# Kernel tuning notes

Measured on AMD Instinct MI355X. Metric: run time of the kernel, lower is better.

Reference implementation:

```python
import jax, jax.numpy as jnp
import numpy as np

B, N, K = 2, 1280, 48
C_NODE, C_EDGE, C_OUT = 384, 128, 128
C_BIAS = C_NODE // 2          # 192 (node_dilation=2)
HID = 2 * C_BIAS + C_EDGE     # 512
LN_EPS = 1e-5


def setup_inputs() -> dict:
    key = jax.random.key(0)
    ks = jax.random.split(key, 13)
    w = lambda k, shape: (jax.random.normal(k, shape, jnp.float32) * 0.02)
    return {
        "node_emb": jax.random.normal(ks[0], (B, N, C_NODE), jnp.float32),
        "edge_emb": jax.random.normal(ks[1], (B, N, K, C_EDGE), jnp.float32),
        "E_idx": jax.random.randint(ks[2], (B, N, K), 0, N),
        "Wi": w(ks[3], (C_NODE, C_BIAS)), "bi": jnp.zeros((C_BIAS,), jnp.float32),
        "W1": w(ks[4], (HID, HID)), "b1": jnp.zeros((HID,), jnp.float32),
        "W2": w(ks[5], (HID, HID)), "b2": jnp.zeros((HID,), jnp.float32),
        "Wf": w(ks[6], (HID, C_OUT)), "bf": jnp.zeros((C_OUT,), jnp.float32),
        "gamma": jnp.ones((C_OUT,), jnp.float32),
        "beta": jnp.zeros((C_OUT,), jnp.float32),
    }


def reference(node_emb, edge_emb, E_idx, Wi, bi, W1, b1, W2, b2, Wf, bf, gamma, beta):
    # initial_embed: [B, N, C_NODE] -> [B, N, C_BIAS]
    n = node_emb @ Wi + bi
    # edge_bias[b,i,k] = concat(n[b,i], n[b, E_idx[b,i,k]])  (tile + gather_edges fused)
    nbr = jax.vmap(lambda v, e: v[e])(n, E_idx)                     # [B, N, K, C_BIAS]
    slf = jnp.broadcast_to(n[:, :, None, :], nbr.shape)             # [B, N, K, C_BIAS]
    x = jnp.concatenate([edge_emb, slf, nbr], axis=-1)              # [B, N, K, HID]
    h = jax.nn.relu(x @ W1 + b1)
    h = jax.nn.relu(h @ W2 + b2)
    # final_layer on residual sum, then LayerNorm
    y = (h + x) @ Wf + bf                                           # [B, N, K, C_OUT]
    mu = jnp.mean(y, axis=-1, keepdims=True)
    var = jnp.mean((y - mu) ** 2, axis=-1, keepdims=True)
    return (y - mu) * jax.lax.rsqrt(var + LN_EPS) * gamma + beta
```

## Files before the change

### kernel.cpp

```cpp
#include <hip/hip_runtime.h>
#include <stdint.h>

#define BB    2
#define NN    1280
#define KK    48
#define CN    384
#define CE    128
#define CB    192
#define HID   512
#define CO    128
#define MM    (BB*NN*KK)
#define CH    (MM/2)

typedef __bf16 bf16x8 __attribute__((ext_vector_type(8)));
typedef float  f32x4  __attribute__((ext_vector_type(4)));
typedef unsigned short u16x8 __attribute__((ext_vector_type(8)));

__device__ __forceinline__ unsigned short f2bf(float f) {
  unsigned int i = __builtin_bit_cast(unsigned int, f);
  unsigned int r = (i + 0x7fffu + ((i >> 16) & 1u)) >> 16;
  return (unsigned short)r;
}
__device__ __forceinline__ float bf2f(unsigned short u) {
  unsigned int v = ((unsigned int)u) << 16;
  return __builtin_bit_cast(float, v);
}

__device__ __forceinline__ void gload_lds16(const void* g, void* l) {
  __builtin_amdgcn_global_load_lds(
      (const __attribute__((address_space(1))) void*)g,
      (__attribute__((address_space(3))) void*)l, 16, 0, 0);
}

__device__ __forceinline__ void mfma_tiles(const char* ldsA, const char* ldsB,
                                           int l, int wm, int wn,
                                           f32x4 (&acc)[4][4]) {
#pragma unroll
  for (int kk = 0; kk < 2; ++kk) {
    bf16x8 av[4], bv[4];
#pragma unroll
    for (int t = 0; t < 4; ++t) {
      const int ra = wm * 64 + t * 16 + (l & 15);
      const int ca = (kk * 4 + (l >> 4)) ^ (ra & 7);
      av[t] = *(const bf16x8*)(ldsA + ra * 128 + ca * 16);
      const int rb = wn * 64 + t * 16 + (l & 15);
      const int cb = (kk * 4 + (l >> 4)) ^ (rb & 7);
      bv[t] = *(const bf16x8*)(ldsB + rb * 128 + cb * 16);
    }
#pragma unroll
    for (int mt = 0; mt < 4; ++mt)
#pragma unroll
      for (int nt = 0; nt < 4; ++nt)
        acc[mt][nt] = __builtin_amdgcn_mfma_f32_16x16x32_bf16(av[mt], bv[nt], acc[mt][nt], 0, 0, 0);
  }
}

__global__ void k_transpose_cast(const float* __restrict__ in,
                                 unsigned short* __restrict__ out,
                                 int R, int C) {
  __shared__ float tile[32][33];
  const int c0 = blockIdx.x * 32, r0 = blockIdx.y * 32;
  const int tx = threadIdx.x, ty = threadIdx.y;
#pragma unroll
  for (int dy = 0; dy < 32; dy += 8)
    tile[ty + dy][tx] = in[(size_t)(r0 + ty + dy) * C + c0 + tx];
  __syncthreads();
#pragma unroll
  for (int dy = 0; dy < 32; dy += 8)
    out[(size_t)(c0 + ty + dy) * R + r0 + tx] = f2bf(tile[tx][ty + dy]);
}

__global__ void k_node(const float* __restrict__ node,
                       const float* __restrict__ Wi,
                       const float* __restrict__ bi,
                       unsigned short* __restrict__ nbuf) {
  __shared__ float row[CN];
  const int blk = blockIdx.x;
  const float* src = node + (size_t)blk * CN;
  for (int c = threadIdx.x; c < CN; c += CB) row[c] = src[c];
  __syncthreads();
  const int t = threadIdx.x;
  float acc = bi[t];
#pragma unroll 8
  for (int c = 0; c < CN; ++c) acc += row[c] * Wi[(size_t)c * CB + t];
  nbuf[(size_t)blk * CB + t] = f2bf(acc);
}

__global__ __launch_bounds__(256, 2)
void k_gemm1(const float* __restrict__ edge,
             const unsigned short* __restrict__ nbuf,
             const int* __restrict__ eidx,
             const unsigned short* __restrict__ Wt,
             const float* __restrict__ bias,
             unsigned short* __restrict__ out,
             int mbase, int b) {
  __shared__ char lds[32768];
  char* ldsA = lds;
  char* ldsB = lds + 16384;
  const int flat = blockIdx.x;
  const int xcd = flat & 7;
  const int p = flat >> 3;
  const int m0 = (xcd * 60 + (p >> 2)) * 128;
  const int n0 = (p & 3) * 128;
  const int tid = threadIdx.x;
  const int l = tid & 63;
  const int w = tid >> 6;
  const int wm = w >> 1, wn = w & 1;
  const int sr = l >> 3, pc = l & 7;
  const int lc = pc ^ sr;

  int rr[4], big[4], nbrg[4];
  size_t mg[4];
#pragma unroll
  for (int ii = 0; ii < 4; ++ii) {
    const int r = (w * 4 + ii) * 8 + sr;
    rr[ii] = r;
    const int m = mbase + m0 + r;
    mg[ii] = (size_t)m;
    big[ii] = m / KK;
    nbrg[ii] = b * NN + eidx[m];
  }

  f32x4 acc[4][4];
#pragma unroll
  for (int i = 0; i < 4; ++i)
#pragma unroll
    for (int j = 0; j < 4; ++j) acc[i][j] = (f32x4){0.f, 0.f, 0.f, 0.f};

#pragma unroll
  for (int k0 = 0; k0 < HID; k0 += 64) {
    uint4 rga[4];
    if (k0 < 128) {
#pragma unroll
      for (int ii = 0; ii < 4; ++ii) {
        const float4* ep = (const float4*)(edge + mg[ii] * CE + k0 + lc * 8);
        float4 x0 = ep[0], x1 = ep[1];
        u16x8 pk;
        pk[0] = f2bf(x0.x); pk[1] = f2bf(x0.y); pk[2] = f2bf(x0.z); pk[3] = f2bf(x0.w);
        pk[4] = f2bf(x1.x); pk[5] = f2bf(x1.y); pk[6] = f2bf(x1.z); pk[7] = f2bf(x1.w);
        rga[ii] = __builtin_bit_cast(uint4, pk);
      }
    }
    __syncthreads();
#pragma unroll
    for (int ii = 0; ii < 4; ++ii) {
      const int i = w * 4 + ii;
      gload_lds16(Wt + (size_t)(n0 + rr[ii]) * HID + k0 + lc * 8, ldsB + i * 1024);
      if (k0 < 128) {
        *(uint4*)(ldsA + i * 1024 + l * 16) = rga[ii];
      } else if (k0 < 320) {
        gload_lds16(nbuf + (size_t)big[ii] * CB + (k0 - 128) + lc * 8, ldsA + i * 1024);
      } else {
        gload_lds16(nbuf + (size_t)nbrg[ii] * CB + (k0 - 320) + lc * 8, ldsA + i * 1024);
      }
    }
    __syncthreads();
    mfma_tiles(ldsA, ldsB, l, wm, wn, acc);
  }

  __syncthreads();
  unsigned short* tile = (unsigned short*)lds;
  const int q = l >> 4, cc = l & 15;
#pragma unroll
  for (int nt = 0; nt < 4; ++nt) {
    const int col = wn * 64 + nt * 16 + cc;
    const float bvv = bias[n0 + col];
    const int cn = col >> 3, cb = col & 7;
#pragma unroll
    for (int mt = 0; mt < 4; ++mt) {
      const int r0_ = wm * 64 + mt * 16 + q * 4;
#pragma unroll
      for (int r = 0; r < 4; ++r) {
        float v = acc[mt][nt][r] + bvv;
        v = v > 0.f ? v : 0.f;
        const int row = r0_ + r;
        tile[row * 128 + ((cn ^ (row & 7)) << 3) + cb] = f2bf(v);
      }
    }
  }
  __syncthreads();
#pragma unroll
  for (int i = 0; i < 8; ++i) {
    const int c = i * 256 + tid;
    const int row = c >> 4, cn = c & 15;
    u16x8 vv = *(const u16x8*)(tile + row * 128 + ((cn ^ (row & 7)) << 3));
    *(u16x8*)(out + (size_t)(m0 + row) * HID + n0 + cn * 8) = vv;
  }
}

__global__ __launch_bounds__(256, 2)
void k_gemm2(const unsigned short* __restrict__ A,
             const unsigned short* __restrict__ Wt,
             const float* __restrict__ bias,
             const float* __restrict__ edge,
             const unsigned short* __restrict__ nbuf,
             const int* __restrict__ eidx,
             unsigned short* __restrict__ out,
             int mbase, int b) {
  __shared__ char lds[32768];
  char* ldsA = lds;
  char* ldsB = lds + 16384;
  const int flat = blockIdx.x;
  const int xcd = flat & 7;
  const int p = flat >> 3;
  const int m0 = (xcd * 60 + (p >> 2)) * 128;
  const int n0 = (p & 3) * 128;
  const int tid = threadIdx.x;
  const int l = tid & 63;
  const int w = tid >> 6;
  const int wm = w >> 1, wn = w & 1;
  const int sr = l >> 3, pc = l & 7;
  const int lc = pc ^ sr;

  f32x4 acc[4][4];
#pragma unroll
  for (int i = 0; i < 4; ++i)
#pragma unroll
    for (int j = 0; j < 4; ++j) acc[i][j] = (f32x4){0.f, 0.f, 0.f, 0.f};

#pragma unroll
  for (int k0 = 0; k0 < HID; k0 += 64) {
    __syncthreads();
#pragma unroll
    for (int ii = 0; ii < 4; ++ii) {
      const int i = w * 4 + ii;
      const int r = i * 8 + sr;
      gload_lds16(A  + (size_t)(m0 + r) * HID + k0 + lc * 8, ldsA + i * 1024);
      gload_lds16(Wt + (size_t)(n0 + r) * HID + k0 + lc * 8, ldsB + i * 1024);
    }
    __syncthreads();
    mfma_tiles(ldsA, ldsB, l, wm, wn, acc);
  }

  __syncthreads();
  unsigned short* tile = (unsigned short*)lds;
  const int q = l >> 4, cc = l & 15;
#pragma unroll
  for (int nt = 0; nt < 4; ++nt) {
    const int col = wn * 64 + nt * 16 + cc;
    const float bvv = bias[n0 + col];
    const int cn = col >> 3, cb = col & 7;
#pragma unroll
    for (int mt = 0; mt < 4; ++mt) {
      const int r0_ = wm * 64 + mt * 16 + q * 4;
#pragma unroll
      for (int r = 0; r < 4; ++r) {
        float v = acc[mt][nt][r] + bvv;
        v = v > 0.f ? v : 0.f;
        const int row = r0_ + r;
        tile[row * 128 + ((cn ^ (row & 7)) << 3) + cb] = f2bf(v);
      }
    }
  }
  __syncthreads();
#pragma unroll
  for (int i = 0; i < 8; ++i) {
    const int c = i * 256 + tid;
    const int row = c >> 4, cn = c & 15;
    u16x8 vv = *(const u16x8*)(tile + row * 128 + ((cn ^ (row & 7)) << 3));
    const int m = mbase + m0 + row;
    float rv[8];
    if (n0 == 0) {
      const float4* ep = (const float4*)(edge + (size_t)m * CE + cn * 8);
      float4 x0 = ep[0], x1 = ep[1];
      rv[0] = x0.x; rv[1] = x0.y; rv[2] = x0.z; rv[3] = x0.w;
      rv[4] = x1.x; rv[5] = x1.y; rv[6] = x1.z; rv[7] = x1.w;
    } else if (n0 == 128) {
      u16x8 xv = *(const u16x8*)(nbuf + (size_t)(m / KK) * CB + cn * 8);
#pragma unroll
      for (int j = 0; j < 8; ++j) rv[j] = bf2f(xv[j]);
    } else if (n0 == 256) {
      u16x8 xv;
      if (cn < 8) {
        xv = *(const u16x8*)(nbuf + (size_t)(m / KK) * CB + 128 + cn * 8);
      } else {
        const int e = eidx[m];
        xv = *(const u16x8*)(nbuf + (size_t)(b * NN + e) * CB + cn * 8 - 64);
      }
#pragma unroll
      for (int j = 0; j < 8; ++j) rv[j] = bf2f(xv[j]);
    } else {
      const int e = eidx[m];
      u16x8 xv = *(const u16x8*)(nbuf + (size_t)(b * NN + e) * CB + 64 + cn * 8);
#pragma unroll
      for (int j = 0; j < 8; ++j) rv[j] = bf2f(xv[j]);
    }
#pragma unroll
    for (int j = 0; j < 8; ++j) vv[j] = f2bf(bf2f(vv[j]) + rv[j]);
    *(u16x8*)(out + (size_t)(m0 + row) * HID + n0 + cn * 8) = vv;
  }
}

__global__ __launch_bounds__(256, 2)
void k_final(const unsigned short* __restrict__ A,
             const unsigned short* __restrict__ Wft,
             const float* __restrict__ bias,
             const float* __restrict__ gamma,
             const float* __restrict__ beta,
             float* __restrict__ out) {
  __shared__ char lds[32768];
  char* ldsA = lds;
  char* ldsB = lds + 16384;
  const int m0 = blockIdx.x * 128;
  const int tid = threadIdx.x;
  const int l = tid & 63;
  const int w = tid >> 6;
  const int sr = l >> 3, pc = l & 7;
  const int lc = pc ^ sr;

  f32x4 acc[2][8];
#pragma unroll
  for (int i = 0; i < 2; ++i)
#pragma unroll
    for (int j = 0; j < 8; ++j) acc[i][j] = (f32x4){0.f, 0.f, 0.f, 0.f};

#pragma unroll
  for (int k0 = 0; k0 < HID; k0 += 64) {
    __syncthreads();
#pragma unroll
    for (int ii = 0; ii < 4; ++ii) {
      const int i = w * 4 + ii;
      const int r = i * 8 + sr;
      gload_lds16(A   + (size_t)(m0 + r) * HID + k0 + lc * 8, ldsA + i * 1024);
      gload_lds16(Wft + (size_t)r * HID + k0 + lc * 8,        ldsB + i * 1024);
    }
    __syncthreads();
#pragma unroll
    for (int kk = 0; kk < 2; ++kk) {
      bf16x8 av[2], bv[8];
#pragma unroll
      for (int t = 0; t < 2; ++t) {
        const int ra = w * 32 + t * 16 + (l & 15);
        const int ca = (kk * 4 + (l >> 4)) ^ (ra & 7);
        av[t] = *(const bf16x8*)(ldsA + ra * 128 + ca * 16);
      }
#pragma unroll
      for (int t = 0; t < 8; ++t) {
        const int rb = t * 16 + (l & 15);
        const int cb = (kk * 4 + (l >> 4)) ^ (rb & 7);
        bv[t] = *(const bf16x8*)(ldsB + rb * 128 + cb * 16);
      }
#pragma unroll
      for (int mt = 0; mt < 2; ++mt)
#pragma unroll
        for (int nt = 0; nt < 8; ++nt)
          acc[mt][nt] = __builtin_amdgcn_mfma_f32_16x16x32_bf16(av[mt], bv[nt], acc[mt][nt], 0, 0, 0);
    }
  }

  const int q = l >> 4, cc = l & 15;
  float gg[8], bb[8], bs[8];
#pragma unroll
  for (int j = 0; j < 8; ++j) {
    const int col = j * 16 + cc;
    gg[j] = gamma[col];
    bb[j] = beta[col];
    bs[j] = bias[col];
  }
#pragma unroll
  for (int mt = 0; mt < 2; ++mt) {
#pragma unroll
    for (int r = 0; r < 4; ++r) {
      float s = 0.f, ss = 0.f;
#pragma unroll
      for (int j = 0; j < 8; ++j) {
        const float v = acc[mt][j][r] + bs[j];
        acc[mt][j][r] = v;
        s += v;
        ss += v * v;
      }
#pragma unroll
      for (int mk = 1; mk < 16; mk <<= 1) {
        s  += __shfl_xor(s, mk, 64);
        ss += __shfl_xor(ss, mk, 64);
      }
      const float mu = s * (1.f / 128.f);
      const float var = ss * (1.f / 128.f) - mu * mu;
      const float rstd = rsqrtf(var + 1e-5f);
      const int row = m0 + w * 32 + mt * 16 + q * 4 + r;
#pragma unroll
      for (int j = 0; j < 8; ++j) {
        const float v = (acc[mt][j][r] - mu) * rstd * gg[j] + bb[j];
        out[(size_t)row * CO + j * 16 + cc] = v;
      }
    }
  }
}

#define O_N    ((size_t)0)
#define O_WT1  ((size_t)0x100000)
#define O_WT2  (O_WT1 + (size_t)0x80000)
#define O_WFT  (O_WT2 + (size_t)0x80000)
#define O_H1   ((size_t)0x300000)
#define O_A    (O_H1 + (size_t)CH * HID * 2)

extern "C" void kernel_launch(void* const* d_in, const int* in_sizes, int n_in,
                              void* d_out, int out_size, void* d_ws, size_t ws_size,
                              hipStream_t stream) {
  const float* node  = (const float*)d_in[0];
  const float* edge  = (const float*)d_in[1];
  const int*   eidx  = (const int*)d_in[2];
  const float* Wi    = (const float*)d_in[3];
  const float* bi    = (const float*)d_in[4];
  const float* W1    = (const float*)d_in[5];
  const float* b1    = (const float*)d_in[6];
  const float* W2    = (const float*)d_in[7];
  const float* b2    = (const float*)d_in[8];
  const float* Wf    = (const float*)d_in[9];
  const float* bfv   = (const float*)d_in[10];
  const float* gamma = (const float*)d_in[11];
  const float* beta  = (const float*)d_in[12];
  float* out = (float*)d_out;

  char* ws = (char*)d_ws;
  unsigned short* nbuf = (unsigned short*)(ws + O_N);
  unsigned short* Wt1  = (unsigned short*)(ws + O_WT1);
  unsigned short* Wt2  = (unsigned short*)(ws + O_WT2);
  unsigned short* Wft  = (unsigned short*)(ws + O_WFT);
  unsigned short* h1   = (unsigned short*)(ws + O_H1);
  unsigned short* abuf = (unsigned short*)(ws + O_A);

  k_transpose_cast<<<dim3(HID / 32, HID / 32), dim3(32, 8), 0, stream>>>(W1, Wt1, HID, HID);
  k_transpose_cast<<<dim3(HID / 32, HID / 32), dim3(32, 8), 0, stream>>>(W2, Wt2, HID, HID);
  k_transpose_cast<<<dim3(CO / 32, HID / 32), dim3(32, 8), 0, stream>>>(Wf, Wft, HID, CO);

  k_node<<<BB * NN, CB, 0, stream>>>(node, Wi, bi, nbuf);

  for (int c = 0; c < 2; ++c) {
    k_gemm1<<<(CH / 128) * 4, 256, 0, stream>>>(edge, nbuf, eidx, Wt1, b1, h1, c * CH, c);
    k_gemm2<<<(CH / 128) * 4, 256, 0, stream>>>(h1, Wt2, b2, edge, nbuf, eidx, abuf, c * CH, c);
    k_final<<<CH / 128, 256, 0, stream>>>(abuf, Wft, bfv, gamma, beta, out + (size_t)c * CH * CO);
  }
}
```

Measured before the change: 394.7 us.

## Double-buffer LDS tiles in all three GEMM kernels to overlap loads with MFMA

Each GEMM kernel now uses two 32KB LDS buffers. The next K-slice is prefetched with direct-to-LDS global loads, plus register loads for the fp32 edge slice in gemm1, while MFMAs run on the current buffer. This cuts the two barriers per K step to one and hides global load latency behind compute. In exchange, LDS per block grows to 64KB, which can reduce occupancy relative to the launch_bounds target of 2 blocks per CU.

```diff
diff --git a/kernel.cpp b/kernel.cpp
--- a/kernel.cpp
+++ b/kernel.cpp
@@ -94,9 +94,7 @@
              const float* __restrict__ bias,
              unsigned short* __restrict__ out,
              int mbase, int b) {
-  __shared__ char lds[32768];
-  char* ldsA = lds;
-  char* ldsB = lds + 16384;
+  __shared__ char lds[65536];
   const int flat = blockIdx.x;
   const int xcd = flat & 7;
   const int p = flat >> 3;
@@ -128,37 +126,59 @@
     for (int j = 0; j < 4; ++j) acc[i][j] = (f32x4){0.f, 0.f, 0.f, 0.f};
 
 #pragma unroll
-  for (int k0 = 0; k0 < HID; k0 += 64) {
-    uint4 rga[4];
-    if (k0 < 128) {
+  for (int ii = 0; ii < 4; ++ii) {
+    const int i = w * 4 + ii;
+    gload_lds16(Wt + (size_t)(n0 + rr[ii]) * HID + lc * 8, lds + 16384 + i * 1024);
+    const float4* ep = (const float4*)(edge + mg[ii] * CE + lc * 8);
+    float4 x0 = ep[0], x1 = ep[1];
+    u16x8 pk;
+    pk[0] = f2bf(x0.x); pk[1] = f2bf(x0.y); pk[2] = f2bf(x0.z); pk[3] = f2bf(x0.w);
+    pk[4] = f2bf(x1.x); pk[5] = f2bf(x1.y); pk[6] = f2bf(x1.z); pk[7] = f2bf(x1.w);
+    *(uint4*)(lds + i * 1024 + l * 16) = __builtin_bit_cast(uint4, pk);
+  }
+  __syncthreads();
+
+#pragma unroll
+  for (int t = 0; t < 8; ++t) {
+    char* base_c = lds + (t & 1) * 32768;
+    char* base_n = lds + ((t & 1) ^ 1) * 32768;
+    const int kn = (t + 1) * 64;
+    float4 e0[4], e1[4];
+    if (t < 7) {
 #pragma unroll
       for (int ii = 0; ii < 4; ++ii) {
-        const float4* ep = (const float4*)(edge + mg[ii] * CE + k0 + lc * 8);
-        float4 x0 = ep[0], x1 = ep[1];
+        const int i = w * 4 + ii;
+        gload_lds16(Wt + (size_t)(n0 + rr[ii]) * HID + kn + lc * 8,
+                    base_n + 16384 + i * 1024);
+        if (kn < 128) {
+          const float4* ep = (const float4*)(edge + mg[ii] * CE + kn + lc * 8);
+          e0[ii] = ep[0];
+          e1[ii] = ep[1];
+        } else if (kn < 320) {
+          gload_lds16(nbuf + (size_t)big[ii] * CB + (kn - 128) + lc * 8,
+                      base_n + i * 1024);
+        } else {
+          gload_lds16(nbuf + (size_t)nbrg[ii] * CB + (kn - 320) + lc * 8,
+                      base_n + i * 1024);
+        }
+      }
+    }
+    mfma_tiles(base_c, base_c + 16384, l, wm, wn, acc);
+    if (t < 7 && kn < 128) {
+#pragma unroll
+      for (int ii = 0; ii < 4; ++ii) {
+        const int i = w * 4 + ii;
         u16x8 pk;
-        pk[0] = f2bf(x0.x); pk[1] = f2bf(x0.y); pk[2] = f2bf(x0.z); pk[3] = f2bf(x0.w);
-        pk[4] = f2bf(x1.x); pk[5] = f2bf(x1.y); pk[6] = f2bf(x1.z); pk[7] = f2bf(x1.w);
-        rga[ii] = __builtin_bit_cast(uint4, pk);
+        pk[0] = f2bf(e0[ii].x); pk[1] = f2bf(e0[ii].y);
+        pk[2] = f2bf(e0[ii].z); pk[3] = f2bf(e0[ii].w);
+        pk[4] = f2bf(e1[ii].x); pk[5] = f2bf(e1[ii].y);
+        pk[6] = f2bf(e1[ii].z); pk[7] = f2bf(e1[ii].w);
+        *(uint4*)(base_n + i * 1024 + l * 16) = __builtin_bit_cast(uint4, pk);
       }
     }
     __syncthreads();
-#pragma unroll
-    for (int ii = 0; ii < 4; ++ii) {
-      const int i = w * 4 + ii;
-      gload_lds16(Wt + (size_t)(n0 + rr[ii]) * HID + k0 + lc * 8, ldsB + i * 1024);
-      if (k0 < 128) {
-        *(uint4*)(ldsA + i * 1024 + l * 16) = rga[ii];
-      } else if (k0 < 320) {
-        gload_lds16(nbuf + (size_t)big[ii] * CB + (k0 - 128) + lc * 8, ldsA + i * 1024);
-      } else {
-        gload_lds16(nbuf + (size_t)nbrg[ii] * CB + (k0 - 320) + lc * 8, ldsA + i * 1024);
-      }
-    }
-    __syncthreads();
-    mfma_tiles(ldsA, ldsB, l, wm, wn, acc);
-  }
-
-  __syncthreads();
+  }
+
   unsigned short* tile = (unsigned short*)lds;
   const int q = l >> 4, cc = l & 15;
 #pragma unroll
@@ -197,9 +217,7 @@
              const int* __restrict__ eidx,
              unsigned short* __restrict__ out,
              int mbase, int b) {
-  __shared__ char lds[32768];
-  char* ldsA = lds;
-  char* ldsB = lds + 16384;
+  __shared__ char lds[65536];
   const int flat = blockIdx.x;
   const int xcd = flat & 7;
   const int p = flat >> 3;
@@ -219,20 +237,32 @@
     for (int j = 0; j < 4; ++j) acc[i][j] = (f32x4){0.f, 0.f, 0.f, 0.f};
 
 #pragma unroll
-  for (int k0 = 0; k0 < HID; k0 += 64) {
+  for (int ii = 0; ii < 4; ++ii) {
+    const int i = w * 4 + ii;
+    const int r = i * 8 + sr;
+    gload_lds16(A  + (size_t)(m0 + r) * HID + lc * 8, lds + i * 1024);
+    gload_lds16(Wt + (size_t)(n0 + r) * HID + lc * 8, lds + 16384 + i * 1024);
+  }
+  __syncthreads();
+
+#pragma unroll
+  for (int t = 0; t < 8; ++t) {
+    char* base_c = lds + (t & 1) * 32768;
+    char* base_n = lds + ((t & 1) ^ 1) * 32768;
+    const int kn = (t + 1) * 64;
+    if (t < 7) {
+#pragma unroll
+      for (int ii = 0; ii < 4; ++ii) {
+        const int i = w * 4 + ii;
+        const int r = i * 8 + sr;
+        gload_lds16(A  + (size_t)(m0 + r) * HID + kn + lc * 8, base_n + i * 1024);
+        gload_lds16(Wt + (size_t)(n0 + r) * HID + kn + lc * 8, base_n + 16384 + i * 1024);
+      }
+    }
+    mfma_tiles(base_c, base_c + 16384, l, wm, wn, acc);
     __syncthreads();
-#pragma unroll
-    for (int ii = 0; ii < 4; ++ii) {
-      const int i = w * 4 + ii;
-      const int r = i * 8 + sr;
-      gload_lds16(A  + (size_t)(m0 + r) * HID + k0 + lc * 8, ldsA + i * 1024);
-      gload_lds16(Wt + (size_t)(n0 + r) * HID + k0 + lc * 8, ldsB + i * 1024);
-    }
-    __syncthreads();
-    mfma_tiles(ldsA, ldsB, l, wm, wn, acc);
-  }
-
-  __syncthreads();
+  }
+
   unsigned short* tile = (unsigned short*)lds;
   const int q = l >> 4, cc = l & 15;
 #pragma unroll
@@ -298,9 +328,7 @@
              const float* __restrict__ gamma,
              const float* __restrict__ beta,
              float* __restrict__ out) {
-  __shared__ char lds[32768];
-  char* ldsA = lds;
-  char* ldsB = lds + 16384;
+  __shared__ char lds[65536];
   const int m0 = blockIdx.x * 128;
   const int tid = threadIdx.x;
   const int l = tid & 63;
@@ -315,30 +343,43 @@
     for (int j = 0; j < 8; ++j) acc[i][j] = (f32x4){0.f, 0.f, 0.f, 0.f};
 
 #pragma unroll
-  for (int k0 = 0; k0 < HID; k0 += 64) {
-    __syncthreads();
-#pragma unroll
-    for (int ii = 0; ii < 4; ++ii) {
-      const int i = w * 4 + ii;
-      const int r = i * 8 + sr;
-      gload_lds16(A   + (size_t)(m0 + r) * HID + k0 + lc * 8, ldsA + i * 1024);
-      gload_lds16(Wft + (size_t)r * HID + k0 + lc * 8,        ldsB + i * 1024);
-    }
-    __syncthreads();
+  for (int ii = 0; ii < 4; ++ii) {
+    const int i = w * 4 + ii;
+    const int r = i * 8 + sr;
+    gload_lds16(A   + (size_t)(m0 + r) * HID + lc * 8, lds + i * 1024);
+    gload_lds16(Wft + (size_t)r * HID + lc * 8,        lds + 16384 + i * 1024);
+  }
+  __syncthreads();
+
+#pragma unroll
+  for (int t = 0; t < 8; ++t) {
+    char* ldsA = lds + (t & 1) * 32768;
+    char* ldsB = ldsA + 16384;
+    char* base_n = lds + ((t & 1) ^ 1) * 32768;
+    const int kn = (t + 1) * 64;
+    if (t < 7) {
+#pragma unroll
+      for (int ii = 0; ii < 4; ++ii) {
+        const int i = w * 4 + ii;
+        const int r = i * 8 + sr;
+        gload_lds16(A   + (size_t)(m0 + r) * HID + kn + lc * 8, base_n + i * 1024);
+        gload_lds16(Wft + (size_t)r * HID + kn + lc * 8,        base_n + 16384 + i * 1024);
+      }
+    }
 #pragma unroll
     for (int kk = 0; kk < 2; ++kk) {
       bf16x8 av[2], bv[8];
 #pragma unroll
-      for (int t = 0; t < 2; ++t) {
-        const int ra = w * 32 + t * 16 + (l & 15);
+      for (int tt = 0; tt < 2; ++tt) {
+        const int ra = w * 32 + tt * 16 + (l & 15);
         const int ca = (kk * 4 + (l >> 4)) ^ (ra & 7);
-        av[t] = *(const bf16x8*)(ldsA + ra * 128 + ca * 16);
-      }
-#pragma unroll
-      for (int t = 0; t < 8; ++t) {
-        const int rb = t * 16 + (l & 15);
+        av[tt] = *(const bf16x8*)(ldsA + ra * 128 + ca * 16);
+      }
+#pragma unroll
+      for (int tt = 0; tt < 8; ++tt) {
+        const int rb = tt * 16 + (l & 15);
         const int cb = (kk * 4 + (l >> 4)) ^ (rb & 7);
-        bv[t] = *(const bf16x8*)(ldsB + rb * 128 + cb * 16);
+        bv[tt] = *(const bf16x8*)(ldsB + rb * 128 + cb * 16);
       }
 #pragma unroll
       for (int mt = 0; mt < 2; ++mt)
@@ -346,6 +387,7 @@
         for (int nt = 0; nt < 8; ++nt)
           acc[mt][nt] = __builtin_amdgcn_mfma_f32_16x16x32_bf16(av[mt], bv[nt], acc[mt][nt], 0, 0, 0);
     }
+    __syncthreads();
   }
 
   const int q = l >> 4, cc = l & 15;
```

Measured after the change: 422.2 us. +7.0%, slower.

## Restructure GEMMs to keep A rows in registers and whole B panel in LDS

Applied to the files above, without the earlier changes.

All three GEMM kernels are rewritten so each wave loads its A-operand rows directly from global memory into registers for the full K=512, and the block's whole 64-column weight panel is staged into 64 KB of LDS once, with a single barrier. This removes the per-K-step sync/reload loop. The final kernel reads weights straight from global memory with no LDS. Tile shapes change to 64x64 (gemm1), 128x64 (gemm2) and 64-row final blocks, and grids grow to match. The risk is heavy register pressure (up to 32 bf16x8 A fragments) and 64 KB LDS limiting occupancy, plus less reuse of A across N tiles.

```diff
diff --git a/kernel.cpp b/kernel.cpp
--- a/kernel.cpp
+++ b/kernel.cpp
@@ -32,29 +32,6 @@
       (__attribute__((address_space(3))) void*)l, 16, 0, 0);
 }
 
-__device__ __forceinline__ void mfma_tiles(const char* ldsA, const char* ldsB,
-                                           int l, int wm, int wn,
-                                           f32x4 (&acc)[4][4]) {
-#pragma unroll
-  for (int kk = 0; kk < 2; ++kk) {
-    bf16x8 av[4], bv[4];
-#pragma unroll
-    for (int t = 0; t < 4; ++t) {
-      const int ra = wm * 64 + t * 16 + (l & 15);
-      const int ca = (kk * 4 + (l >> 4)) ^ (ra & 7);
-      av[t] = *(const bf16x8*)(ldsA + ra * 128 + ca * 16);
-      const int rb = wn * 64 + t * 16 + (l & 15);
-      const int cb = (kk * 4 + (l >> 4)) ^ (rb & 7);
-      bv[t] = *(const bf16x8*)(ldsB + rb * 128 + cb * 16);
-    }
-#pragma unroll
-    for (int mt = 0; mt < 4; ++mt)
-#pragma unroll
-      for (int nt = 0; nt < 4; ++nt)
-        acc[mt][nt] = __builtin_amdgcn_mfma_f32_16x16x32_bf16(av[mt], bv[nt], acc[mt][nt], 0, 0, 0);
-  }
-}
-
 __global__ void k_transpose_cast(const float* __restrict__ in,
                                  unsigned short* __restrict__ out,
                                  int R, int C) {
@@ -86,6 +63,7 @@
   nbuf[(size_t)blk * CB + t] = f2bf(acc);
 }
 
+
 __global__ __launch_bounds__(256, 2)
 void k_gemm1(const float* __restrict__ edge,
              const unsigned short* __restrict__ nbuf,
@@ -94,96 +72,96 @@
              const float* __restrict__ bias,
              unsigned short* __restrict__ out,
              int mbase, int b) {
-  __shared__ char lds[32768];
-  char* ldsA = lds;
-  char* ldsB = lds + 16384;
+  __shared__ char lds[65536];
   const int flat = blockIdx.x;
   const int xcd = flat & 7;
   const int p = flat >> 3;
-  const int m0 = (xcd * 60 + (p >> 2)) * 128;
-  const int n0 = (p & 3) * 128;
+  const int m0 = (xcd * 120 + (p >> 3)) * 64;
+  const int n0 = (p & 7) * 64;
   const int tid = threadIdx.x;
   const int l = tid & 63;
   const int w = tid >> 6;
-  const int wm = w >> 1, wn = w & 1;
   const int sr = l >> 3, pc = l & 7;
-  const int lc = pc ^ sr;
-
-  int rr[4], big[4], nbrg[4];
-  size_t mg[4];
-#pragma unroll
-  for (int ii = 0; ii < 4; ++ii) {
-    const int r = (w * 4 + ii) * 8 + sr;
-    rr[ii] = r;
-    const int m = mbase + m0 + r;
-    mg[ii] = (size_t)m;
-    big[ii] = m / KK;
-    nbrg[ii] = b * NN + eidx[m];
-  }
-
-  f32x4 acc[4][4];
-#pragma unroll
-  for (int i = 0; i < 4; ++i)
-#pragma unroll
-    for (int j = 0; j < 4; ++j) acc[i][j] = (f32x4){0.f, 0.f, 0.f, 0.f};
-
-#pragma unroll
-  for (int k0 = 0; k0 < HID; k0 += 64) {
-    uint4 rga[4];
-    if (k0 < 128) {
-#pragma unroll
-      for (int ii = 0; ii < 4; ++ii) {
-        const float4* ep = (const float4*)(edge + mg[ii] * CE + k0 + lc * 8);
-        float4 x0 = ep[0], x1 = ep[1];
-        u16x8 pk;
-        pk[0] = f2bf(x0.x); pk[1] = f2bf(x0.y); pk[2] = f2bf(x0.z); pk[3] = f2bf(x0.w);
-        pk[4] = f2bf(x1.x); pk[5] = f2bf(x1.y); pk[6] = f2bf(x1.z); pk[7] = f2bf(x1.w);
-        rga[ii] = __builtin_bit_cast(uint4, pk);
-      }
-    }
-    __syncthreads();
-#pragma unroll
-    for (int ii = 0; ii < 4; ++ii) {
-      const int i = w * 4 + ii;
-      gload_lds16(Wt + (size_t)(n0 + rr[ii]) * HID + k0 + lc * 8, ldsB + i * 1024);
-      if (k0 < 128) {
-        *(uint4*)(ldsA + i * 1024 + l * 16) = rga[ii];
-      } else if (k0 < 320) {
-        gload_lds16(nbuf + (size_t)big[ii] * CB + (k0 - 128) + lc * 8, ldsA + i * 1024);
-      } else {
-        gload_lds16(nbuf + (size_t)nbrg[ii] * CB + (k0 - 320) + lc * 8, ldsA + i * 1024);
-      }
-    }
-    __syncthreads();
-    mfma_tiles(ldsA, ldsB, l, wm, wn, acc);
+  const int kg = l >> 4, lr = l & 15;
+
+  const int m = mbase + m0 + w * 16 + lr;
+  const int big = m / KK;
+  const int nbr = b * NN + eidx[m];
+  const float* ep = edge + (size_t)m * CE + kg * 8;
+  float4 ed0[4], ed1[4];
+#pragma unroll
+  for (int s = 0; s < 4; ++s) {
+    ed0[s] = *(const float4*)(ep + s * 32);
+    ed1[s] = *(const float4*)(ep + s * 32 + 4);
+  }
+  const unsigned short* sp = nbuf + (size_t)big * CB + kg * 8;
+  const unsigned short* np = nbuf + (size_t)nbr * CB + kg * 8;
+  bf16x8 sf[6], nb[6];
+#pragma unroll
+  for (int s = 0; s < 6; ++s) sf[s] = *(const bf16x8*)(sp + s * 32);
+#pragma unroll
+  for (int s = 0; s < 6; ++s) nb[s] = *(const bf16x8*)(np + s * 32);
+
+#pragma unroll
+  for (int ww = 0; ww < 2; ++ww) {
+    const int win = w * 2 + ww;
+#pragma unroll
+    for (int j = 0; j < 8; ++j)
+      gload_lds16(Wt + (size_t)(n0 + j * 8 + sr) * HID + win * 64 + (pc ^ sr) * 8,
+                  lds + win * 8192 + j * 1024);
+  }
+  __syncthreads();
+
+  f32x4 acc[4];
+#pragma unroll
+  for (int nt = 0; nt < 4; ++nt) acc[nt] = (f32x4){0.f, 0.f, 0.f, 0.f};
+
+#pragma unroll
+  for (int s = 0; s < 16; ++s) {
+    bf16x8 av;
+    if (s < 4) {
+      u16x8 pk;
+      pk[0] = f2bf(ed0[s].x); pk[1] = f2bf(ed0[s].y);
+      pk[2] = f2bf(ed0[s].z); pk[3] = f2bf(ed0[s].w);
+      pk[4] = f2bf(ed1[s].x); pk[5] = f2bf(ed1[s].y);
+      pk[6] = f2bf(ed1[s].z); pk[7] = f2bf(ed1[s].w);
+      av = __builtin_bit_cast(bf16x8, pk);
+    } else if (s < 10) {
+      av = sf[s - 4];
+    } else {
+      av = nb[s - 10];
+    }
+    const char* bwin = lds + (s >> 1) * 8192;
+    const int kk = s & 1;
+#pragma unroll
+    for (int nt = 0; nt < 4; ++nt) {
+      const int rb = nt * 16 + lr;
+      const bf16x8 bv = *(const bf16x8*)(bwin + rb * 128 + (((kk << 2) + kg) ^ (rb & 7)) * 16);
+      acc[nt] = __builtin_amdgcn_mfma_f32_16x16x32_bf16(av, bv, acc[nt], 0, 0, 0);
+    }
   }
 
   __syncthreads();
   unsigned short* tile = (unsigned short*)lds;
-  const int q = l >> 4, cc = l & 15;
 #pragma unroll
   for (int nt = 0; nt < 4; ++nt) {
-    const int col = wn * 64 + nt * 16 + cc;
+    const int col = nt * 16 + lr;
     const float bvv = bias[n0 + col];
     const int cn = col >> 3, cb = col & 7;
 #pragma unroll
-    for (int mt = 0; mt < 4; ++mt) {
-      const int r0_ = wm * 64 + mt * 16 + q * 4;
-#pragma unroll
-      for (int r = 0; r < 4; ++r) {
-        float v = acc[mt][nt][r] + bvv;
-        v = v > 0.f ? v : 0.f;
-        const int row = r0_ + r;
-        tile[row * 128 + ((cn ^ (row & 7)) << 3) + cb] = f2bf(v);
-      }
-    }
-  }
-  __syncthreads();
-#pragma unroll
-  for (int i = 0; i < 8; ++i) {
+    for (int r = 0; r < 4; ++r) {
+      float v = acc[nt][r] + bvv;
+      v = v > 0.f ? v : 0.f;
+      const int row = w * 16 + kg * 4 + r;
+      tile[row * 64 + ((cn ^ (row & 7)) << 3) + cb] = f2bf(v);
+    }
+  }
+  __syncthreads();
+#pragma unroll
+  for (int i = 0; i < 2; ++i) {
     const int c = i * 256 + tid;
-    const int row = c >> 4, cn = c & 15;
-    u16x8 vv = *(const u16x8*)(tile + row * 128 + ((cn ^ (row & 7)) << 3));
+    const int row = c >> 3, cn = c & 7;
+    u16x8 vv = *(const u16x8*)(tile + row * 64 + ((cn ^ (row & 7)) << 3));
     *(u16x8*)(out + (size_t)(m0 + row) * HID + n0 + cn * 8) = vv;
   }
 }
@@ -197,91 +175,94 @@
              const int* __restrict__ eidx,
              unsigned short* __restrict__ out,
              int mbase, int b) {
-  __shared__ char lds[32768];
-  char* ldsA = lds;
-  char* ldsB = lds + 16384;
+  __shared__ char lds[65536];
   const int flat = blockIdx.x;
   const int xcd = flat & 7;
   const int p = flat >> 3;
-  const int m0 = (xcd * 60 + (p >> 2)) * 128;
-  const int n0 = (p & 3) * 128;
+  const int m0 = (xcd * 60 + (p >> 3)) * 128;
+  const int n0 = (p & 7) * 64;
   const int tid = threadIdx.x;
   const int l = tid & 63;
   const int w = tid >> 6;
-  const int wm = w >> 1, wn = w & 1;
   const int sr = l >> 3, pc = l & 7;
-  const int lc = pc ^ sr;
-
-  f32x4 acc[4][4];
-#pragma unroll
-  for (int i = 0; i < 4; ++i)
-#pragma unroll
-    for (int j = 0; j < 4; ++j) acc[i][j] = (f32x4){0.f, 0.f, 0.f, 0.f};
-
-#pragma unroll
-  for (int k0 = 0; k0 < HID; k0 += 64) {
-    __syncthreads();
-#pragma unroll
-    for (int ii = 0; ii < 4; ++ii) {
-      const int i = w * 4 + ii;
-      const int r = i * 8 + sr;
-      gload_lds16(A  + (size_t)(m0 + r) * HID + k0 + lc * 8, ldsA + i * 1024);
-      gload_lds16(Wt + (size_t)(n0 + r) * HID + k0 + lc * 8, ldsB + i * 1024);
-    }
-    __syncthreads();
-    mfma_tiles(ldsA, ldsB, l, wm, wn, acc);
+  const int kg = l >> 4, lr = l & 15;
+
+  bf16x8 areg[2][16];
+#pragma unroll
+  for (int t = 0; t < 2; ++t) {
+    const unsigned short* ap = A + (size_t)(m0 + w * 32 + t * 16 + lr) * HID + kg * 8;
+#pragma unroll
+    for (int s = 0; s < 16; ++s) areg[t][s] = *(const bf16x8*)(ap + s * 32);
+  }
+#pragma unroll
+  for (int ww = 0; ww < 2; ++ww) {
+    const int win = w * 2 + ww;
+#pragma unroll
+    for (int j = 0; j < 8; ++j)
+      gload_lds16(Wt + (size_t)(n0 + j * 8 + sr) * HID + win * 64 + (pc ^ sr) * 8,
+                  lds + win * 8192 + j * 1024);
+  }
+  __syncthreads();
+
+  f32x4 acc[2][4];
+#pragma unroll
+  for (int t = 0; t < 2; ++t)
+#pragma unroll
+    for (int nt = 0; nt < 4; ++nt) acc[t][nt] = (f32x4){0.f, 0.f, 0.f, 0.f};
+
+#pragma unroll
+  for (int s = 0; s < 16; ++s) {
+    const char* bwin = lds + (s >> 1) * 8192;
+    const int kk = s & 1;
+    bf16x8 bv[4];
+#pragma unroll
+    for (int nt = 0; nt < 4; ++nt) {
+      const int rb = nt * 16 + lr;
+      bv[nt] = *(const bf16x8*)(bwin + rb * 128 + (((kk << 2) + kg) ^ (rb & 7)) * 16);
+    }
+#pragma unroll
+    for (int t = 0; t < 2; ++t)
+#pragma unroll
+      for (int nt = 0; nt < 4; ++nt)
+        acc[t][nt] = __builtin_amdgcn_mfma_f32_16x16x32_bf16(areg[t][s], bv[nt], acc[t][nt], 0, 0, 0);
   }
 
   __syncthreads();
   unsigned short* tile = (unsigned short*)lds;
-  const int q = l >> 4, cc = l & 15;
-#pragma unroll
-  for (int nt = 0; nt < 4; ++nt) {
-    const int col = wn * 64 + nt * 16 + cc;
-    const float bvv = bias[n0 + col];
-    const int cn = col >> 3, cb = col & 7;
-#pragma unroll
-    for (int mt = 0; mt < 4; ++mt) {
-      const int r0_ = wm * 64 + mt * 16 + q * 4;
+#pragma unroll
+  for (int t = 0; t < 2; ++t)
+#pragma unroll
+    for (int nt = 0; nt < 4; ++nt) {
+      const int col = nt * 16 + lr;
+      const float bvv = bias[n0 + col];
+      const int cn = col >> 3, cb = col & 7;
 #pragma unroll
       for (int r = 0; r < 4; ++r) {
-        float v = acc[mt][nt][r] + bvv;
+        float v = acc[t][nt][r] + bvv;
         v = v > 0.f ? v : 0.f;
-        const int row = r0_ + r;
-        tile[row * 128 + ((cn ^ (row & 7)) << 3) + cb] = f2bf(v);
+        const int row = w * 32 + t * 16 + kg * 4 + r;
+        tile[row * 64 + ((cn ^ (row & 7)) << 3) + cb] = f2bf(v);
       }
     }
-  }
-  __syncthreads();
-#pragma unroll
-  for (int i = 0; i < 8; ++i) {
+  __syncthreads();
+#pragma unroll
+  for (int i = 0; i < 4; ++i) {
     const int c = i * 256 + tid;
-    const int row = c >> 4, cn = c & 15;
-    u16x8 vv = *(const u16x8*)(tile + row * 128 + ((cn ^ (row & 7)) << 3));
-    const int m = mbase + m0 + row;
+    const int row = c >> 3, cn = c & 7;
+    u16x8 vv = *(const u16x8*)(tile + row * 64 + ((cn ^ (row & 7)) << 3));
+    const int mm = mbase + m0 + row;
     float rv[8];
-    if (n0 == 0) {
-      const float4* ep = (const float4*)(edge + (size_t)m * CE + cn * 8);
-      float4 x0 = ep[0], x1 = ep[1];
+    if (n0 < 128) {
+      const float4* rp = (const float4*)(edge + (size_t)mm * CE + n0 + cn * 8);
+      float4 x0 = rp[0], x1 = rp[1];
       rv[0] = x0.x; rv[1] = x0.y; rv[2] = x0.z; rv[3] = x0.w;
       rv[4] = x1.x; rv[5] = x1.y; rv[6] = x1.z; rv[7] = x1.w;
-    } else if (n0 == 128) {
-      u16x8 xv = *(const u16x8*)(nbuf + (size_t)(m / KK) * CB + cn * 8);
-#pragma unroll
-      for (int j = 0; j < 8; ++j) rv[j] = bf2f(xv[j]);
-    } else if (n0 == 256) {
-      u16x8 xv;
-      if (cn < 8) {
-        xv = *(const u16x8*)(nbuf + (size_t)(m / KK) * CB + 128 + cn * 8);
-      } else {
-        const int e = eidx[m];
-        xv = *(const u16x8*)(nbuf + (size_t)(b * NN + e) * CB + cn * 8 - 64);
-      }
+    } else if (n0 < 320) {
+      u16x8 xv = *(const u16x8*)(nbuf + (size_t)(mm / KK) * CB + (n0 - 128) + cn * 8);
 #pragma unroll
       for (int j = 0; j < 8; ++j) rv[j] = bf2f(xv[j]);
     } else {
-      const int e = eidx[m];
-      u16x8 xv = *(const u16x8*)(nbuf + (size_t)(b * NN + e) * CB + 64 + cn * 8);
+      u16x8 xv = *(const u16x8*)(nbuf + (size_t)(b * NN + eidx[mm]) * CB + (n0 - 320) + cn * 8);
 #pragma unroll
       for (int j = 0; j < 8; ++j) rv[j] = bf2f(xv[j]);
     }
@@ -298,91 +279,64 @@
              const float* __restrict__ gamma,
              const float* __restrict__ beta,
              float* __restrict__ out) {
-  __shared__ char lds[32768];
-  char* ldsA = lds;
-  char* ldsB = lds + 16384;
-  const int m0 = blockIdx.x * 128;
+  const int flat = blockIdx.x;
+  const int xcd = flat & 7;
+  const int p = flat >> 3;
+  const int m0 = (xcd * 120 + p) * 64;
   const int tid = threadIdx.x;
   const int l = tid & 63;
   const int w = tid >> 6;
-  const int sr = l >> 3, pc = l & 7;
-  const int lc = pc ^ sr;
-
-  f32x4 acc[2][8];
-#pragma unroll
-  for (int i = 0; i < 2; ++i)
-#pragma unroll
-    for (int j = 0; j < 8; ++j) acc[i][j] = (f32x4){0.f, 0.f, 0.f, 0.f};
-
-#pragma unroll
-  for (int k0 = 0; k0 < HID; k0 += 64) {
-    __syncthreads();
-#pragma unroll
-    for (int ii = 0; ii < 4; ++ii) {
-      const int i = w * 4 + ii;
-      const int r = i * 8 + sr;
-      gload_lds16(A   + (size_t)(m0 + r) * HID + k0 + lc * 8, ldsA + i * 1024);
-      gload_lds16(Wft + (size_t)r * HID + k0 + lc * 8,        ldsB + i * 1024);
-    }
-    __syncthreads();
-#pragma unroll
-    for (int kk = 0; kk < 2; ++kk) {
-      bf16x8 av[2], bv[8];
-#pragma unroll
-      for (int t = 0; t < 2; ++t) {
-        const int ra = w * 32 + t * 16 + (l & 15);
-        const int ca = (kk * 4 + (l >> 4)) ^ (ra & 7);
-        av[t] = *(const bf16x8*)(ldsA + ra * 128 + ca * 16);
-      }
-#pragma unroll
-      for (int t = 0; t < 8; ++t) {
-        const int rb = t * 16 + (l & 15);
-        const int cb = (kk * 4 + (l >> 4)) ^ (rb & 7);
-        bv[t] = *(const bf16x8*)(ldsB + rb * 128 + cb * 16);
-      }
-#pragma unroll
-      for (int mt = 0; mt < 2; ++mt)
-#pragma unroll
-        for (int nt = 0; nt < 8; ++nt)
-          acc[mt][nt] = __builtin_amdgcn_mfma_f32_16x16x32_bf16(av[mt], bv[nt], acc[mt][nt], 0, 0, 0);
-    }
-  }
-
-  const int q = l >> 4, cc = l & 15;
+  const int kg = l >> 4, lr = l & 15;
+
+  bf16x8 areg[16];
+  const unsigned short* ap = A + (size_t)(m0 + w * 16 + lr) * HID + kg * 8;
+#pragma unroll
+  for (int s = 0; s < 16; ++s) areg[s] = *(const bf16x8*)(ap + s * 32);
+
+  f32x4 acc[8];
+#pragma unroll
+  for (int j = 0; j < 8; ++j) acc[j] = (f32x4){0.f, 0.f, 0.f, 0.f};
+
+#pragma unroll
+  for (int s = 0; s < 16; ++s) {
+#pragma unroll
+    for (int nt = 0; nt < 8; ++nt) {
+      const bf16x8 bv = *(const bf16x8*)(Wft + (size_t)(nt * 16 + lr) * HID + s * 32 + kg * 8);
+      acc[nt] = __builtin_amdgcn_mfma_f32_16x16x32_bf16(areg[s], bv, acc[nt], 0, 0, 0);
+    }
+  }
+
   float gg[8], bb[8], bs[8];
 #pragma unroll
   for (int j = 0; j < 8; ++j) {
-    const int col = j * 16 + cc;
+    const int col = j * 16 + lr;
     gg[j] = gamma[col];
     bb[j] = beta[col];
     bs[j] = bias[col];
   }
 #pragma unroll
-  for (int mt = 0; mt < 2; ++mt) {
-#pragma unroll
-    for (int r = 0; r < 4; ++r) {
-      float s = 0.f, ss = 0.f;
-#pragma unroll
-      for (int j = 0; j < 8; ++j) {
-        const float v = acc[mt][j][r] + bs[j];
-        acc[mt][j][r] = v;
-        s += v;
-        ss += v * v;
-      }
-#pragma unroll
-      for (int mk = 1; mk < 16; mk <<= 1) {
-        s  += __shfl_xor(s, mk, 64);
-        ss += __shfl_xor(ss, mk, 64);
-      }
-      const float mu = s * (1.f / 128.f);
-      const float var = ss * (1.f / 128.f) - mu * mu;
-      const float rstd = rsqrtf(var + 1e-5f);
-      const int row = m0 + w * 32 + mt * 16 + q * 4 + r;
-#pragma unroll
-      for (int j = 0; j < 8; ++j) {
-        const float v = (acc[mt][j][r] - mu) * rstd * gg[j] + bb[j];
-        out[(size_t)row * CO + j * 16 + cc] = v;
-      }
+  for (int r = 0; r < 4; ++r) {
+    float s = 0.f, ss = 0.f;
+#pragma unroll
+    for (int j = 0; j < 8; ++j) {
+      const float v = acc[j][r] + bs[j];
+      acc[j][r] = v;
+      s += v;
+      ss += v * v;
+    }
+#pragma unroll
+    for (int mk = 1; mk < 16; mk <<= 1) {
+      s  += __shfl_xor(s, mk, 64);
+      ss += __shfl_xor(ss, mk, 64);
+    }
+    const float mu = s * (1.f / 128.f);
+    const float var = ss * (1.f / 128.f) - mu * mu;
+    const float rstd = rsqrtf(var + 1e-5f);
+    const int row = m0 + w * 16 + kg * 4 + r;
+#pragma unroll
+    for (int j = 0; j < 8; ++j) {
+      const float v = (acc[j][r] - mu) * rstd * gg[j] + bb[j];
+      out[(size_t)row * CO + j * 16 + lr] = v;
     }
   }
 }
@@ -427,8 +381,8 @@
   k_node<<<BB * NN, CB, 0, stream>>>(node, Wi, bi, nbuf);
 
   for (int c = 0; c < 2; ++c) {
-    k_gemm1<<<(CH / 128) * 4, 256, 0, stream>>>(edge, nbuf, eidx, Wt1, b1, h1, c * CH, c);
-    k_gemm2<<<(CH / 128) * 4, 256, 0, stream>>>(h1, Wt2, b2, edge, nbuf, eidx, abuf, c * CH, c);
-    k_final<<<CH / 128, 256, 0, stream>>>(abuf, Wft, bfv, gamma, beta, out + (size_t)c * CH * CO);
-  }
-}
+    k_gemm1<<<(CH / 64) * 8, 256, 0, stream>>>(edge, nbuf, eidx, Wt1, b1, h1, c * CH, c);
+    k_gemm2<<<(CH / 128) * 8, 256, 0, stream>>>(h1, Wt2, b2, edge, nbuf, eidx, abuf, c * CH, c);
+    k_final<<<CH / 64, 256, 0, stream>>>(abuf, Wft, bfv, gamma, beta, out + (size_t)c * CH * CO);
+  }
+}
```

After: 678.1 us. +71.8%, slower.

## Stage full Wf in LDS and hold A rows in registers for final GEMM

Applied to the files above, without the earlier changes.

The final GEMM+LayerNorm kernel now loads the whole transposed Wf (128x512 bf16, 128KB) into LDS once per block. Each wave loads its 32 rows of A straight from global memory into registers, so the per-k-step barrier loop is gone. This removes the repeated syncthreads and LDS staging of A. The cost is 128KB of LDS and more registers, which limits occupancy to one block per CU (launch bounds changed to 1).

```diff
diff --git a/kernel.cpp b/kernel.cpp
--- a/kernel.cpp
+++ b/kernel.cpp
@@ -291,74 +291,71 @@
   }
 }
 
-__global__ __launch_bounds__(256, 2)
+__global__ __launch_bounds__(256, 1)
 void k_final(const unsigned short* __restrict__ A,
              const unsigned short* __restrict__ Wft,
              const float* __restrict__ bias,
              const float* __restrict__ gamma,
              const float* __restrict__ beta,
              float* __restrict__ out) {
-  __shared__ char lds[32768];
-  char* ldsA = lds;
-  char* ldsB = lds + 16384;
+  __shared__ char lds[131072];
   const int m0 = blockIdx.x * 128;
   const int tid = threadIdx.x;
-  const int l = tid & 63;
-  const int w = tid >> 6;
+  const int l = tid & 63, w = tid >> 6;
   const int sr = l >> 3, pc = l & 7;
   const int lc = pc ^ sr;
-
-  f32x4 acc[2][8];
-#pragma unroll
-  for (int i = 0; i < 2; ++i)
-#pragma unroll
-    for (int j = 0; j < 8; ++j) acc[i][j] = (f32x4){0.f, 0.f, 0.f, 0.f};
-
-#pragma unroll
-  for (int k0 = 0; k0 < HID; k0 += 64) {
-    __syncthreads();
-#pragma unroll
-    for (int ii = 0; ii < 4; ++ii) {
-      const int i = w * 4 + ii;
-      const int r = i * 8 + sr;
-      gload_lds16(A   + (size_t)(m0 + r) * HID + k0 + lc * 8, ldsA + i * 1024);
-      gload_lds16(Wft + (size_t)r * HID + k0 + lc * 8,        ldsB + i * 1024);
-    }
-    __syncthreads();
-#pragma unroll
-    for (int kk = 0; kk < 2; ++kk) {
-      bf16x8 av[2], bv[8];
-#pragma unroll
-      for (int t = 0; t < 2; ++t) {
-        const int ra = w * 32 + t * 16 + (l & 15);
-        const int ca = (kk * 4 + (l >> 4)) ^ (ra & 7);
-        av[t] = *(const bf16x8*)(ldsA + ra * 128 + ca * 16);
-      }
-#pragma unroll
-      for (int t = 0; t < 8; ++t) {
-        const int rb = t * 16 + (l & 15);
-        const int cb = (kk * 4 + (l >> 4)) ^ (rb & 7);
-        bv[t] = *(const bf16x8*)(ldsB + rb * 128 + cb * 16);
-      }
-#pragma unroll
-      for (int mt = 0; mt < 2; ++mt)
-#pragma unroll
-        for (int nt = 0; nt < 8; ++nt)
-          acc[mt][nt] = __builtin_amdgcn_mfma_f32_16x16x32_bf16(av[mt], bv[nt], acc[mt][nt], 0, 0, 0);
-    }
-  }
-
-  const int q = l >> 4, cc = l & 15;
+  const int kg = l >> 4, lr = l & 15;
+
+#pragma unroll
+  for (int ww = 0; ww < 2; ++ww) {
+    const int win = w * 2 + ww;
+#pragma unroll
+    for (int j = 0; j < 16; ++j)
+      gload_lds16(Wft + (size_t)(j * 8 + sr) * HID + win * 64 + lc * 8,
+                  lds + win * 16384 + j * 1024);
+  }
+
+  bf16x8 alo[16], ahi[16];
+  {
+    const unsigned short* a0 = A + (size_t)(m0 + w * 32 + lr) * HID + kg * 8;
+    const unsigned short* a1 = A + (size_t)(m0 + w * 32 + 16 + lr) * HID + kg * 8;
+#pragma unroll
+    for (int s = 0; s < 16; ++s) {
+      alo[s] = *(const bf16x8*)(a0 + s * 32);
+      ahi[s] = *(const bf16x8*)(a1 + s * 32);
+    }
+  }
+
   float gg[8], bb[8], bs[8];
 #pragma unroll
   for (int j = 0; j < 8; ++j) {
-    const int col = j * 16 + cc;
+    const int col = j * 16 + lr;
     gg[j] = gamma[col];
     bb[j] = beta[col];
     bs[j] = bias[col];
   }
-#pragma unroll
-  for (int mt = 0; mt < 2; ++mt) {
+  __syncthreads();
+
+  f32x4 acc[2][8];
+#pragma unroll
+  for (int mt = 0; mt < 2; ++mt)
+#pragma unroll
+    for (int nt = 0; nt < 8; ++nt) acc[mt][nt] = (f32x4){0.f, 0.f, 0.f, 0.f};
+
+#pragma unroll
+  for (int s = 0; s < 16; ++s) {
+    const char* bwin = lds + (s >> 1) * 16384;
+#pragma unroll
+    for (int nt = 0; nt < 8; ++nt) {
+      const int rb = nt * 16 + lr;
+      const bf16x8 bv = *(const bf16x8*)(bwin + rb * 128 + ((((s & 1) << 2) + kg) ^ (rb & 7)) * 16);
+      acc[0][nt] = __builtin_amdgcn_mfma_f32_16x16x32_bf16(alo[s], bv, acc[0][nt], 0, 0, 0);
+      acc[1][nt] = __builtin_amdgcn_mfma_f32_16x16x32_bf16(ahi[s], bv, acc[1][nt], 0, 0, 0);
+    }
+  }
+
+#pragma unroll
+  for (int mt = 0; mt < 2; ++mt)
 #pragma unroll
     for (int r = 0; r < 4; ++r) {
       float s = 0.f, ss = 0.f;
@@ -377,14 +374,13 @@
       const float mu = s * (1.f / 128.f);
       const float var = ss * (1.f / 128.f) - mu * mu;
       const float rstd = rsqrtf(var + 1e-5f);
-      const int row = m0 + w * 32 + mt * 16 + q * 4 + r;
+      const int row = m0 + w * 32 + mt * 16 + kg * 4 + r;
 #pragma unroll
       for (int j = 0; j < 8; ++j) {
         const float v = (acc[mt][j][r] - mu) * rstd * gg[j] + bb[j];
-        out[(size_t)row * CO + j * 16 + cc] = v;
-      }
-    }
-  }
+        out[(size_t)row * CO + j * 16 + lr] = v;
+      }
+    }
 }
 
 #define O_N    ((size_t)0)
```

Result: slower. 417.3 us (+5.7%).
